# Kernel tuning notes

Hardware: AMD Instinct MI355X
Metric: run time of the kernel (lower is better)

The kernel has to match this reference:

```python
import jax, jax.numpy as jnp
import numpy as np

DEPTH, DIM, HEADS, DIM_HEAD, NBF, MULT = 2, 512, 8, 64, 256, 4
INNER = HEADS * DIM_HEAD


def layernorm(x, g, b, eps=1e-5):
    mu = jnp.mean(x, axis=-1, keepdims=True)
    var = jnp.mean((x - mu) ** 2, axis=-1, keepdims=True)
    return (x - mu) * jax.lax.rsqrt(var + eps) * g + b


def softmax_kernel(data, proj, is_query, eps=1e-4):
    # data: [b,h,n,d], proj: [m,d]  -> phi: [b,h,n,m]  (FAVOR+ positive features)
    d = data.shape[-1]
    normalizer = d ** -0.25
    ratio = proj.shape[0] ** -0.5
    data_dash = jnp.einsum('bhnd,md->bhnm', data * normalizer, proj)
    diag = jnp.sum(data ** 2, axis=-1, keepdims=True) * 0.5 * (normalizer ** 2)
    if is_query:
        m = jnp.max(data_dash, axis=-1, keepdims=True)
    else:
        m = jnp.max(data_dash, axis=(-2, -1), keepdims=True)
    m = jax.lax.stop_gradient(m)
    return ratio * (jnp.exp(data_dash - diag - m) + eps)


def setup_inputs() -> dict:
    key = jax.random.key(0)
    ks = jax.random.split(key, 16)
    s = 0.02
    B, N = 4, 8192
    inp = {
        'x': jax.random.normal(ks[0], (B, N, DIM), jnp.float32),
        'ln1_g': jnp.ones((DEPTH, DIM), jnp.float32),
        'ln1_b': jnp.zeros((DEPTH, DIM), jnp.float32),
        'ln2_g': jnp.ones((DEPTH, DIM), jnp.float32),
        'ln2_b': jnp.zeros((DEPTH, DIM), jnp.float32),
        'Wq': jax.random.normal(ks[1], (DEPTH, DIM, INNER), jnp.float32) * s,
        'bq': jnp.zeros((DEPTH, INNER), jnp.float32),
        'Wk': jax.random.normal(ks[2], (DEPTH, DIM, INNER), jnp.float32) * s,
        'bk': jnp.zeros((DEPTH, INNER), jnp.float32),
        'Wv': jax.random.normal(ks[3], (DEPTH, DIM, INNER), jnp.float32) * s,
        'bv': jnp.zeros((DEPTH, INNER), jnp.float32),
        'Wo': jax.random.normal(ks[4], (DEPTH, INNER, DIM), jnp.float32) * s,
        'bo': jnp.zeros((DEPTH, DIM), jnp.float32),
        'proj': jax.random.normal(ks[5], (DEPTH, NBF, DIM_HEAD), jnp.float32),
        'W1': jax.random.normal(ks[6], (DEPTH, DIM, DIM * MULT), jnp.float32) * s,
        'b1': jnp.zeros((DEPTH, DIM * MULT), jnp.float32),
        'W2': jax.random.normal(ks[7], (DEPTH, DIM * MULT, DIM), jnp.float32) * s,
        'b2': jnp.zeros((DEPTH, DIM), jnp.float32),
    }
    return inp


def reference(x, ln1_g, ln1_b, ln2_g, ln2_b, Wq, bq, Wk, bk, Wv, bv, Wo, bo, proj, W1, b1, W2, b2):
    B, N, D = x.shape
    for i in range(DEPTH):
        # --- PreLayerNorm + FAVOR+ self-attention, residual ---
        y = layernorm(x, ln1_g[i], ln1_b[i])
        q = (y @ Wq[i] + bq[i]).reshape(B, N, HEADS, DIM_HEAD).transpose(0, 2, 1, 3)
        k = (y @ Wk[i] + bk[i]).reshape(B, N, HEADS, DIM_HEAD).transpose(0, 2, 1, 3)
        v = (y @ Wv[i] + bv[i]).reshape(B, N, HEADS, DIM_HEAD).transpose(0, 2, 1, 3)
        qp = softmax_kernel(q, proj[i], True)   # [b,h,n,m]
        kp = softmax_kernel(k, proj[i], False)  # [b,h,n,m]
        # non-causal linear attention: O(n*m*d) instead of O(n^2)
        k_sum = kp.sum(axis=2)                               # [b,h,m]
        d_inv = 1.0 / jnp.einsum('bhnm,bhm->bhn', qp, k_sum)
        ctx = jnp.einsum('bhnm,bhnd->bhmd', kp, v)           # [b,h,m,d]
        o = jnp.einsum('bhmd,bhnm,bhn->bhnd', ctx, qp, d_inv)
        o = o.transpose(0, 2, 1, 3).reshape(B, N, INNER)
        x = x + o @ Wo[i] + bo[i]
        # --- PreLayerNorm + FeedForward (GELU), residual ---
        y = layernorm(x, ln2_g[i], ln2_b[i])
        h = jax.nn.gelu(y @ W1[i] + b1[i], approximate=False)
        x = x + h @ W2[i] + b2[i]
    return x
```

## Files before the change

### kernel.cpp

```cpp
#include <hip/hip_runtime.h>
#include <math.h>

#define DIMX 512
#define HEADS 8
#define DHEAD 64
#define NBFX 256
#define FFD 2048
#define NBX 4
#define SEQ 8192
#define TOK (NBX*SEQ)
#define NBH (NBX*HEADS)
#define VROWS 80
#define NCHUNK 16
#define BK 64

typedef unsigned short u16;
typedef __attribute__((ext_vector_type(8))) short short8;
typedef __attribute__((ext_vector_type(4))) float f32x4;

__device__ __forceinline__ float bf2f(u16 x){ return __uint_as_float(((unsigned)x)<<16); }
__device__ __forceinline__ u16 f2bf(float f){
  unsigned u=__float_as_uint(f);
  return (u16)((u + 0x7FFFu + ((u>>16)&1u))>>16);
}
__device__ __forceinline__ void gload16(const void* g, void* l){
  __builtin_amdgcn_global_load_lds((const __attribute__((address_space(1))) void*)g,
                                   (__attribute__((address_space(3))) void*)l, 16, 0, 0);
}
__device__ __forceinline__ float gelu_f(float v){
  float x=v*0.70710678118654752f;
  float ax=fabsf(x);
  float t=1.0f/(1.0f+0.3275911f*ax);
  float p=t*(0.254829592f+t*(-0.284496736f+t*(1.421413741f+t*(-1.453152027f+t*1.061405429f))));
  float erfv=1.0f-p*__expf(-ax*ax);
  erfv=(x<0.0f)? -erfv : erfv;
  return 0.5f*v*(1.0f+erfv);
}

#define FENCE asm volatile(""::: "memory")
#define BAR() do{ FENCE; __builtin_amdgcn_s_barrier(); FENCE; }while(0)

__global__ void copy_f32(const float4* __restrict__ s, float4* __restrict__ d, int n4){
  int i=blockIdx.x*blockDim.x+threadIdx.x;
  if(i<n4) d[i]=s[i];
}
__global__ void conv_proj(const float* __restrict__ p, u16* __restrict__ o, int n){
  int i=blockIdx.x*blockDim.x+threadIdx.x;
  if(i<n) o[i]=f2bf(p[i]*0.35355339059327373f);
}
__global__ void convT(const float* __restrict__ src, u16* __restrict__ dst, int K, int Ncol){
  __shared__ float t[32][33];
  int k0=blockIdx.y*32, n0=blockIdx.x*32;
  int tx=threadIdx.x, ty=threadIdx.y;
  for(int i=ty;i<32;i+=8) t[i][tx]=src[(size_t)(k0+i)*Ncol + n0+tx];
  __syncthreads();
  for(int i=ty;i<32;i+=8) dst[(size_t)(n0+i)*K + k0+tx]=f2bf(t[tx][i]);
}
__global__ void fill_vt(u16* __restrict__ vt){
  int i=blockIdx.x*blockDim.x+threadIdx.x;
  int n=i&(SEQ-1); int r=(i>>13)&15; int bh=i>>17;
  vt[((size_t)bh*VROWS + 64 + r)*SEQ + n] = (r==0)? (u16)0x3F80 : (u16)0;
}
__global__ void pack_bias(const float* __restrict__ bq, const float* __restrict__ bk,
                          const float* __restrict__ bv, float* __restrict__ o){
  int i=blockIdx.x*blockDim.x+threadIdx.x;
  int l=i/1536, c=i-l*1536;
  const float* s=(c<512)? bq : ((c<1024)? bk : bv);
  o[i]=s[l*512 + (c&511)];
}

__global__ __launch_bounds__(256) void ln_k(const float* __restrict__ x, const float* __restrict__ g,
                                            const float* __restrict__ b, u16* __restrict__ y){
  const int row=blockIdx.x*4 + (threadIdx.x>>6);
  const int ln=threadIdx.x&63;
  const float* xr=x+(size_t)row*DIMX;
  float4 v0=*(const float4*)&xr[ln*8];
  float4 v1=*(const float4*)&xr[ln*8+4];
  float v[8]={v0.x,v0.y,v0.z,v0.w,v1.x,v1.y,v1.z,v1.w};
  float s=0;
  #pragma unroll
  for(int e=0;e<8;e++) s+=v[e];
  #pragma unroll
  for(int m=1;m<64;m<<=1) s+=__shfl_xor(s,m);
  const float mean=s*(1.0f/DIMX);
  float s2=0;
  #pragma unroll
  for(int e=0;e<8;e++){ v[e]-=mean; s2+=v[e]*v[e]; }
  #pragma unroll
  for(int m=1;m<64;m<<=1) s2+=__shfl_xor(s2,m);
  const float rs=rsqrtf(s2*(1.0f/DIMX)+1e-5f);
  u16* yr=y+(size_t)row*DIMX+ln*8;
  u16 pk[8];
  #pragma unroll
  for(int e=0;e<8;e++) pk[e]=f2bf(v[e]*rs*g[ln*8+e]+b[ln*8+e]);
  uint4 pv;
  pv.x=(unsigned)pk[0]|((unsigned)pk[1]<<16); pv.y=(unsigned)pk[2]|((unsigned)pk[3]<<16);
  pv.z=(unsigned)pk[4]|((unsigned)pk[5]<<16); pv.w=(unsigned)pk[6]|((unsigned)pk[7]<<16);
  *(uint4*)yr=pv;
}

#define MFMA16(MH,BF,NH) do{                                                             \
  __builtin_amdgcn_s_setprio(1);                                                         \
  _Pragma("unroll") for(int kk_=0;kk_<2;kk_++)                                           \
    _Pragma("unroll") for(int i_=0;i_<4;i_++)                                            \
      _Pragma("unroll") for(int j_=0;j_<2;j_++)                                          \
        acc[MH][i_][NH][j_]=__builtin_amdgcn_mfma_f32_16x16x32_bf16(af[i_][kk_],BF[j_][kk_],acc[MH][i_][NH][j_],0,0,0); \
  __builtin_amdgcn_s_setprio(0);                                                         \
}while(0)

#define STG(T,HALF,ISB,BUF) do{ if((T)<nt){                                              \
  gload16(gp[ISB][HALF][0]+(size_t)(T)*BK, &lds[BUF][ISB][(HALF)*128 +    wv*8][0]);     \
  gload16(gp[ISB][HALF][1]+(size_t)(T)*BK, &lds[BUF][ISB][(HALF)*128 + 64+wv*8][0]); } }while(0)

#define LDA(BUF,MH) do{                                                                  \
  _Pragma("unroll") for(int i_=0;i_<4;i_++)                                              \
    _Pragma("unroll") for(int kk_=0;kk_<2;kk_++)                                         \
      af[i_][kk_]=*(const short8*)((const u16*)lds[BUF][0] + aoffs[MH][i_][kk_]); }while(0)

#define LDB(BF,BUF,NH) do{                                                               \
  _Pragma("unroll") for(int j_=0;j_<2;j_++)                                              \
    _Pragma("unroll") for(int kk_=0;kk_<2;kk_++)                                         \
      BF[j_][kk_]=*(const short8*)((const u16*)lds[BUF][1] + boffs[NH][j_][kk_]); }while(0)

#define TILE(T,BUF,OBUF) do{                                                             \
  LDB(bf0,BUF,0); LDA(BUF,0);                                                            \
  STG((T)+1,1,0,OBUF);                                                                   \
  BAR(); MFMA16(0,bf0,0); BAR();                                                         \
  LDB(bf1,BUF,1);                                                                        \
  STG((T)+1,1,1,OBUF);                                                                   \
  BAR(); MFMA16(0,bf1,1); BAR();                                                         \
  LDA(BUF,1);                                                                            \
  STG((T)+2,0,1,BUF);                                                                    \
  BAR(); MFMA16(1,bf0,0); BAR();                                                         \
  STG((T)+2,0,0,BUF);                                                                    \
  BAR(); MFMA16(1,bf1,1);                                                                \
  if((T)+2<nt) asm volatile("s_waitcnt vmcnt(4)":::"memory");                            \
  else         asm volatile("s_waitcnt vmcnt(0)":::"memory");                            \
  BAR();                                                                                 \
}while(0)

template<int EPI,int K>
__global__ __launch_bounds__(512,2) void gemm256(const u16* __restrict__ A, const u16* __restrict__ Bt,
                                                 const float* __restrict__ bias, void* __restrict__ outp,
                                                 u16* __restrict__ out2, int Ncol){
  constexpr int nt=K/BK;
  __shared__ u16 lds[2][2][256][64];
  const int tid=threadIdx.x, wv=tid>>6, ln=tid&63;
  const int wr=wv>>2, wc=wv&3;
  const int gx=gridDim.x, gy=gridDim.y;
  const int P=blockIdx.y*gx+blockIdx.x;
  const int band=gy>>3;
  const int xcd=P&7, sI=P>>3;
  const int by=xcd*band + (sI - (sI/band)*band);
  const int bx=sI/band;
  const int m0=by*256, n0=bx*256;
  f32x4 acc[2][4][2][2]={};

  const u16* gp[2][2][2];
  #pragma unroll
  for(int isB=0;isB<2;isB++)
    #pragma unroll
    for(int half=0;half<2;half++)
      #pragma unroll
      for(int s=0;s<2;s++){
        int G=s*512+wv*64+ln;
        int arow=half*128+(G>>3), g=G&7;
        const u16* src=isB? Bt:A;
        int b0=isB? n0:m0;
        gp[isB][half][s]=src+(size_t)(b0+arow)*K+((g^(arow&7))<<3);
      }
  int aoffs[2][4][2], boffs[2][2][2];
  #pragma unroll
  for(int mh=0;mh<2;mh++)
    #pragma unroll
    for(int i=0;i<4;i++){
      int row=wr*128+mh*64+i*16+(ln&15);
      #pragma unroll
      for(int kk=0;kk<2;kk++)
        aoffs[mh][i][kk]=row*64+((((kk*4+(ln>>4)))^(row&7))<<3);
    }
  #pragma unroll
  for(int nh=0;nh<2;nh++)
    #pragma unroll
    for(int j=0;j<2;j++){
      int row=wc*64+nh*32+j*16+(ln&15);
      #pragma unroll
      for(int kk=0;kk<2;kk++)
        boffs[nh][j][kk]=row*64+((((kk*4+(ln>>4)))^(row&7))<<3);
    }

  short8 af[4][2], bf0[2][2], bf1[2][2];

  STG(0,0,0,0); STG(0,1,0,0); STG(0,0,1,0); STG(0,1,1,0);
  STG(1,0,1,1); STG(1,0,0,1);
  asm volatile("s_waitcnt vmcnt(4)":::"memory");
  BAR();

  #pragma unroll 1
  for(int t=0;t<nt;t+=2){
    TILE(t,0,1);
    TILE(t+1,1,0);
  }

  #pragma unroll
  for(int mh=0;mh<2;mh++)
  #pragma unroll
  for(int i=0;i<4;i++)
  #pragma unroll
  for(int nh=0;nh<2;nh++)
  #pragma unroll
  for(int j=0;j<2;j++){
    const int row=m0+wr*128+mh*64+i*16+(ln>>4)*4;
    const int col=n0+wc*64+nh*32+j*16+(ln&15);
    const float bv=bias[col];
    const f32x4 a=acc[mh][i][nh][j];
    if constexpr(EPI==0){
      if(col<1024){
        u16* o=(u16*)outp + (size_t)(col>>9)*TOK*DIMX + (col&511);
        #pragma unroll
        for(int r=0;r<4;r++) o[(size_t)(row+r)*DIMX]=f2bf(a[r]+bv);
      } else {
        const int hd=col-1024, h_=hd>>6, d_=hd&63, b_=row>>13, nn=row&(SEQ-1);
        u16 pk[4];
        #pragma unroll
        for(int r=0;r<4;r++) pk[r]=f2bf(a[r]+bv);
        uint2 pv; pv.x=(unsigned)pk[0]|((unsigned)pk[1]<<16); pv.y=(unsigned)pk[2]|((unsigned)pk[3]<<16);
        *(uint2*)&out2[((size_t)(b_*HEADS+h_)*VROWS+d_)*SEQ+nn]=pv;
      }
    } else if constexpr(EPI==1){
      float* o=(float*)outp;
      #pragma unroll
      for(int r=0;r<4;r++){ size_t ix=(size_t)(row+r)*Ncol+col; o[ix]+=a[r]+bv; }
    } else {
      u16* o=(u16*)outp;
      #pragma unroll
      for(int r=0;r<4;r++)
        o[(size_t)(row+r)*Ncol+col]=f2bf(gelu_f(a[r]+bv));
    }
  }
}

__global__ __launch_bounds__(256) void vsum_k(const u16* __restrict__ vt, float* __restrict__ vs){
  const int gw=blockIdx.x*4 + (threadIdx.x>>6);
  const int ln=threadIdx.x&63;
  const int bh=gw/65, d=gw-bh*65;
  const u16* row=vt+((size_t)bh*VROWS+d)*SEQ;
  float s=0;
  for(int it=0;it<16;it++){
    short8 v=*(const short8*)&row[it*512+ln*8];
    #pragma unroll
    for(int e=0;e<8;e++) s+=bf2f((u16)v[e]);
  }
  #pragma unroll
  for(int m=1;m<64;m<<=1) s+=__shfl_xor(s,m);
  if(ln==0) vs[bh*80+d]=s;
}

__global__ __launch_bounds__(256) void kctx(const u16* __restrict__ kb, const u16* __restrict__ pj,
                                            const u16* __restrict__ vt,
                                            float* __restrict__ part, float* __restrict__ maxb){
  __shared__ u16 kl[64*64];
  __shared__ u16 vl[80*64];
  __shared__ u16 kp_l[128*64];
  __shared__ float dgl[64];
  const int kc=blockIdx.x, half=blockIdx.y, bh=blockIdx.z, b_=bh>>3, h_=bh&7;
  const int tid=threadIdx.x, wv=tid>>6, ln=tid&63;
  short8 pjf[2][2];
  #pragma unroll
  for(int i=0;i<2;i++)
    #pragma unroll
    for(int t=0;t<2;t++)
      pjf[i][t]=*(const short8*)&pj[(size_t)(half*128+wv*32+i*16+(ln&15))*DHEAD + t*32 + (ln>>4)*8];
  f32x4 ctx[2][5]={};
  float m_run=-3.0e38f;
  const u16* vbh=vt+(size_t)bh*VROWS*SEQ;
  for(int s=0;s<8;s++){
    const int n0s=kc*512+s*64;
    const u16* kg=kb+((size_t)(b_*SEQ+n0s))*DIMX + h_*DHEAD;
    #pragma unroll
    for(int cc=0;cc<2;cc++){
      int c=cc*256+wv*64+ln; int t=c>>3, g=c&7;
      gload16(kg+(size_t)t*DIMX+((g^(t&7))*8), &kl[(size_t)(cc*256+wv*64)*8]);
    }
    #pragma unroll
    for(int cc=0;cc<2;cc++){
      int c=cc*256+wv*64+ln; int d=c>>3, g=c&7;
      gload16(vbh+(size_t)d*SEQ+n0s+((g^(d&7))*8), &vl[(size_t)(cc*256+wv*64)*8]);
    }
    if(wv<2){
      int c=512+wv*64+ln; int d=c>>3, g=c&7;
      gload16(vbh+(size_t)d*SEQ+n0s+((g^(d&7))*8), &vl[(size_t)(512+wv*64)*8]);
    }
    __syncthreads();
    if(tid<64){
      float ss=0;
      #pragma unroll
      for(int gg=0;gg<8;gg++){
        short8 kv=*(const short8*)&kl[tid*64 + ((gg+tid)&7)*8];
        #pragma unroll
        for(int e=0;e<8;e++){ float x=bf2f((u16)kv[e]); ss+=x*x; }
      }
      dgl[tid]=ss*0.0625f;
    }
    __syncthreads();
    f32x4 dd[2][4]={};
    #pragma unroll
    for(int tk=0;tk<2;tk++)
      #pragma unroll
      for(int j=0;j<4;j++){
        short8 bk_=*(const short8*)&kl[(j*16+(ln&15))*64 + (((tk*4+(ln>>4))^(ln&7))<<3)];
        #pragma unroll
        for(int i=0;i<2;i++)
          dd[i][j]=__builtin_amdgcn_mfma_f32_16x16x32_bf16(pjf[i][tk],bk_,dd[i][j],0,0,0);
      }
    float mt=-3.0e38f;
    #pragma unroll
    for(int i=0;i<2;i++)
      #pragma unroll
      for(int j=0;j<4;j++)
        #pragma unroll
        for(int r=0;r<4;r++) mt=fmaxf(mt,dd[i][j][r]);
    #pragma unroll
    for(int m=1;m<64;m<<=1) mt=fmaxf(mt,__shfl_xor(mt,m));
    if(mt>m_run){
      float sc=__expf(m_run-mt);
      #pragma unroll
      for(int i=0;i<2;i++)
        #pragma unroll
        for(int j2=0;j2<5;j2++) ctx[i][j2]*=sc;
      m_run=mt;
    }
    #pragma unroll
    for(int j=0;j<4;j++){
      const float dgn=dgl[j*16+(ln&15)];
      #pragma unroll
      for(int i=0;i<2;i++)
        #pragma unroll
        for(int r=0;r<4;r++){
          int m_l=wv*32+i*16+(ln>>4)*4+r;
          float E=__expf(dd[i][j][r]-dgn-m_run);
          kp_l[m_l*64 + (((j*2+((ln>>3)&1))^(m_l&7))<<3) + (ln&7)]=f2bf(E);
        }
    }
    #pragma unroll
    for(int tk=0;tk<2;tk++){
      short8 af2[2];
      #pragma unroll
      for(int i=0;i<2;i++)
        af2[i]=*(const short8*)&kp_l[(wv*32+i*16+(ln&15))*64 + (((tk*4+(ln>>4))^(ln&7))<<3)];
      #pragma unroll
      for(int j2=0;j2<5;j2++){
        short8 bf2=*(const short8*)&vl[(j2*16+(ln&15))*64 + (((tk*4+(ln>>4))^(ln&7))<<3)];
        #pragma unroll
        for(int i=0;i<2;i++)
          ctx[i][j2]=__builtin_amdgcn_mfma_f32_16x16x32_bf16(af2[i],bf2,ctx[i][j2],0,0,0);
      }
    }
    __syncthreads();
  }
  float* po=part + ((size_t)(bh*NCHUNK+kc))*(256*80) + (size_t)half*128*80;
  #pragma unroll
  for(int i=0;i<2;i++)
    #pragma unroll
    for(int j2=0;j2<5;j2++)
      #pragma unroll
      for(int r=0;r<4;r++)
        po[(size_t)(wv*32+i*16+(ln>>4)*4+r)*80 + j2*16+(ln&15)]=ctx[i][j2][r];
  if(ln==0) maxb[bh*128 + kc*8 + half*4 + wv]=m_run;
}

__global__ __launch_bounds__(256) void ctx_reduce(const float* __restrict__ part, const float* __restrict__ maxb,
                                                  const float* __restrict__ vs,
                                                  u16* __restrict__ ctxT, float* __restrict__ ksum){
  __shared__ float mx_s[128];
  __shared__ float sc_s[NCHUNK];
  const int mseg=blockIdx.x, bh=blockIdx.y, tid=threadIdx.x;
  if(tid<128) mx_s[tid]=maxb[(size_t)bh*128+tid];
  __syncthreads();
  float km=-3.0e38f;
  for(int i=0;i<128;i++) km=fmaxf(km,mx_s[i]);
  const int m0=mseg*32;
  const int half=m0>>7, wvv=(m0&127)>>5;
  if(tid<NCHUNK) sc_s[tid]=__expf(mx_s[tid*8+half*4+wvv]-km);
  __syncthreads();
  for(int rep=0;rep<10;rep++){
    int idx=rep*256+tid;
    int mo=idx/80, d=idx-mo*80;
    int m=m0+mo;
    float s=0;
    #pragma unroll
    for(int c=0;c<NCHUNK;c++)
      s+=sc_s[c]*part[((size_t)(bh*NCHUNK+c))*(256*80) + (size_t)m*80 + d];
    float vsd=(d<=64)? vs[bh*80+d] : 0.0f;
    float val=0.0625f*(s + 1e-4f*vsd);
    if(d<64)       ctxT[((size_t)bh*64+d)*NBFX + m]=f2bf(val);
    else if(d==64) ksum[bh*NBFX+m]=val;
  }
}

__global__ void csum_k(const u16* __restrict__ ctxT, const float* __restrict__ ksum, float* __restrict__ cs){
  const int bh=blockIdx.x, t=threadIdx.x;
  if(t<64){
    const u16* r=ctxT+((size_t)bh*64+t)*NBFX;
    float s=0;
    for(int m=0;m<NBFX;m+=8){
      short8 v=*(const short8*)&r[m];
      #pragma unroll
      for(int e=0;e<8;e++) s+=bf2f((u16)v[e]);
    }
    cs[bh*80+t]=s;
  } else if(t==64){
    float s=0;
    for(int m=0;m<NBFX;m++) s+=ksum[bh*NBFX+m];
    cs[bh*80+64]=s;
  }
}

__global__ __launch_bounds__(256) void q_fused(const u16* __restrict__ qb, const u16* __restrict__ pj,
                                               const u16* __restrict__ ctxT, const float* __restrict__ ksum,
                                               const float* __restrict__ cs, u16* __restrict__ ob){
  __shared__ u16 ql[64*64];
  __shared__ u16 qpl[64*136];
  __shared__ float dgs[64];
  __shared__ float mred[4*64], dred[4*64];
  __shared__ float ff_s[64], dinv_s[64];
  const int bh=blockIdx.y, b_=bh>>3, h_=bh&7;
  const int n0=blockIdx.x*64;
  const int tid=threadIdx.x, wv=tid>>6, ln=tid&63;
  const u16* qg=qb+((size_t)(b_*SEQ+n0))*DIMX + h_*DHEAD;
  #pragma unroll
  for(int cc=0;cc<2;cc++){
    int c=cc*256+wv*64+ln; int t=c>>3, g=c&7;
    gload16(qg+(size_t)t*DIMX+((g^(t&7))*8), &ql[(size_t)(cc*256+wv*64)*8]);
  }
  short8 pjf[2][2][2];
  float ks[2][2][4];
  #pragma unroll
  for(int h=0;h<2;h++)
    #pragma unroll
    for(int i=0;i<2;i++){
      #pragma unroll
      for(int t=0;t<2;t++)
        pjf[h][i][t]=*(const short8*)&pj[(size_t)(h*128+wv*32+i*16+(ln&15))*DHEAD + t*32 + (ln>>4)*8];
      #pragma unroll
      for(int r=0;r<4;r++)
        ks[h][i][r]=ksum[bh*NBFX + h*128+wv*32+i*16+(ln>>4)*4+r];
    }
  const float KS=cs[bh*80+64];
  __syncthreads();
  if(tid<64){
    float ss=0;
    #pragma unroll
    for(int gg=0;gg<8;gg++){
      short8 kv=*(const short8*)&ql[tid*64 + ((gg+tid)&7)*8];
      #pragma unroll
      for(int e=0;e<8;e++){ float x=bf2f((u16)kv[e]); ss+=x*x; }
    }
    dgs[tid]=ss*0.0625f;
  }
  __syncthreads();
  float mxp[4]={-3.0e38f,-3.0e38f,-3.0e38f,-3.0e38f};
  float dnp[4]={0,0,0,0};
  f32x4 oc[4]={};
  const u16* cb=ctxT+(size_t)bh*64*NBFX;
  #pragma unroll
  for(int h=0;h<2;h++){
    #pragma unroll
    for(int j=0;j<4;j++){
      f32x4 dq[2]={};
      #pragma unroll
      for(int tk=0;tk<2;tk++){
        short8 bq=*(const short8*)&ql[(j*16+(ln&15))*64 + (((tk*4+(ln>>4))^(ln&7))<<3)];
        #pragma unroll
        for(int i=0;i<2;i++)
          dq[i]=__builtin_amdgcn_mfma_f32_16x16x32_bf16(pjf[h][i][tk],bq,dq[i],0,0,0);
      }
      const float dgn=dgs[j*16+(ln&15)];
      #pragma unroll
      for(int i=0;i<2;i++)
        #pragma unroll
        for(int r=0;r<4;r++){
          float d_=dq[i][r];
          mxp[j]=fmaxf(mxp[j],d_);
          float E=__expf(d_-dgn);
          dnp[j]+=E*ks[h][i][r];
          qpl[(j*16+(ln&15))*136 + wv*32+i*16+(ln>>4)*4+r]=f2bf(E);
        }
    }
    __syncthreads();
    #pragma unroll
    for(int mk2=0;mk2<4;mk2++){
      short8 aq=*(const short8*)&cb[(size_t)(wv*16+(ln&15))*NBFX + h*128 + mk2*32 + (ln>>4)*8];
      #pragma unroll
      for(int j2=0;j2<4;j2++){
        short8 bqp=*(const short8*)&qpl[(j2*16+(ln&15))*136 + mk2*32 + (ln>>4)*8];
        oc[j2]=__builtin_amdgcn_mfma_f32_16x16x32_bf16(aq,bqp,oc[j2],0,0,0);
      }
    }
    __syncthreads();
  }
  #pragma unroll
  for(int j=0;j<4;j++){
    #pragma unroll
    for(int msk=16;msk<64;msk<<=1){
      mxp[j]=fmaxf(mxp[j],__shfl_xor(mxp[j],msk));
      dnp[j]+=__shfl_xor(dnp[j],msk);
    }
  }
  if(ln<16){
    #pragma unroll
    for(int j=0;j<4;j++){ mred[wv*64+j*16+ln]=mxp[j]; dred[wv*64+j*16+ln]=dnp[j]; }
  }
  __syncthreads();
  if(tid<64){
    float mx=fmaxf(fmaxf(mred[tid],mred[64+tid]),fmaxf(mred[128+tid],mred[192+tid]));
    float dn=dred[tid]+dred[64+tid]+dred[128+tid]+dred[192+tid];
    float f=1e-4f*__expf(mx);
    ff_s[tid]=f;
    dinv_s[tid]=1.0f/(dn + f*KS);
  }
  __syncthreads();
  float csr[4];
  #pragma unroll
  for(int r=0;r<4;r++) csr[r]=cs[bh*80 + wv*16+(ln>>4)*4+r];
  u16* og=ob+((size_t)(b_*SEQ+n0))*DIMX + h_*DHEAD;
  #pragma unroll
  for(int j2=0;j2<4;j2++){
    int n=j2*16+(ln&15);
    float f=ff_s[n], di=dinv_s[n];
    u16 pk[4];
    #pragma unroll
    for(int r=0;r<4;r++) pk[r]=f2bf((oc[j2][r]+f*csr[r])*di);
    uint2 pv; pv.x=(unsigned)pk[0]|((unsigned)pk[1]<<16); pv.y=(unsigned)pk[2]|((unsigned)pk[3]<<16);
    *(uint2*)&og[(size_t)n*DIMX + wv*16+(ln>>4)*4]=pv;
  }
}

static constexpr size_t SZ_ACT=(size_t)TOK*DIMX*2;
static constexpr size_t O_Y=0, O_Q=SZ_ACT, O_K=2*SZ_ACT;
static constexpr size_t O_VT=3*SZ_ACT;
static constexpr size_t SZ_VT=(size_t)NBH*VROWS*SEQ*2;
static constexpr size_t O_PART=O_VT+SZ_VT;
static constexpr size_t SZ_PART=(size_t)NBH*NCHUNK*256*80*4;
static constexpr size_t O_CTXT=O_PART+SZ_PART;
static constexpr size_t SZ_CTXT=(size_t)NBH*64*NBFX*2;
static constexpr size_t O_KSUM=O_CTXT+SZ_CTXT;
static constexpr size_t SZ_KSUM=(size_t)NBH*NBFX*4;
static constexpr size_t O_MAX=O_KSUM+SZ_KSUM;
static constexpr size_t SZ_MAX=(size_t)NBH*128*4;
static constexpr size_t O_VSUM=O_MAX+SZ_MAX;
static constexpr size_t SZ_VSUM=(size_t)NBH*80*4;
static constexpr size_t O_CS=O_VSUM+SZ_VSUM;
static constexpr size_t SZ_CS=(size_t)NBH*80*4;
static constexpr size_t O_WQKV=O_CS+SZ_CS;
static constexpr size_t SZ_WQKV=(size_t)2*1536*DIMX*2;
static constexpr size_t O_WOT=O_WQKV+SZ_WQKV;
static constexpr size_t SZ_W=(size_t)2*DIMX*DIMX*2;
static constexpr size_t O_W1T=O_WOT+SZ_W;
static constexpr size_t SZ_W1=(size_t)2*FFD*DIMX*2;
static constexpr size_t O_W2T=O_W1T+SZ_W1;
static constexpr size_t O_PJ=O_W2T+SZ_W1;
static constexpr size_t O_QKVB=O_PJ+(size_t)2*NBFX*DHEAD*2;
static constexpr size_t WS_END=O_QKVB+(size_t)2*1536*4;

extern "C" void kernel_launch(void* const* d_in, const int* in_sizes, int n_in,
                              void* d_out, int out_size, void* d_ws, size_t ws_size,
                              hipStream_t stream){
  (void)in_sizes;(void)n_in;(void)out_size;
  const float* xin =(const float*)d_in[0];
  const float* ln1g=(const float*)d_in[1];
  const float* ln1b=(const float*)d_in[2];
  const float* ln2g=(const float*)d_in[3];
  const float* ln2b=(const float*)d_in[4];
  const float* Wq=(const float*)d_in[5];
  const float* bq=(const float*)d_in[6];
  const float* Wk=(const float*)d_in[7];
  const float* bk=(const float*)d_in[8];
  const float* Wv=(const float*)d_in[9];
  const float* bv=(const float*)d_in[10];
  const float* Wo=(const float*)d_in[11];
  const float* bo=(const float*)d_in[12];
  const float* proj=(const float*)d_in[13];
  const float* W1=(const float*)d_in[14];
  const float* b1=(const float*)d_in[15];
  const float* W2=(const float*)d_in[16];
  const float* b2=(const float*)d_in[17];
  float* xout=(float*)d_out;

  copy_f32<<<(TOK*DIMX/4)/256,256,0,stream>>>((const float4*)xin,(float4*)xout, TOK*DIMX/4);
  if(ws_size < WS_END) return;

  char* ws=(char*)d_ws;
  u16* ybuf =(u16*)(ws+O_Y);
  u16* qbuf =(u16*)(ws+O_Q);
  u16* kbuf =(u16*)(ws+O_K);
  u16* vtb  =(u16*)(ws+O_VT);
  float* partb=(float*)(ws+O_PART);
  u16* ctxtb=(u16*)(ws+O_CTXT);
  float* ksumb=(float*)(ws+O_KSUM);
  float* maxb=(float*)(ws+O_MAX);
  float* vsumb=(float*)(ws+O_VSUM);
  float* csb=(float*)(ws+O_CS);
  u16* wqkvt=(u16*)(ws+O_WQKV);
  u16* wot=(u16*)(ws+O_WOT);
  u16* w1t=(u16*)(ws+O_W1T); u16* w2t=(u16*)(ws+O_W2T);
  u16* pjb=(u16*)(ws+O_PJ);
  float* qkvb=(float*)(ws+O_QKVB);
  u16* hbuf=(u16*)(ws+O_Q);

  for(int l=0;l<2;l++){
    size_t wo=(size_t)l*DIMX*DIMX;
    convT<<<dim3(16,16),dim3(32,8),0,stream>>>(Wq+wo, wqkvt+(size_t)(l*1536+   0)*DIMX, DIMX, DIMX);
    convT<<<dim3(16,16),dim3(32,8),0,stream>>>(Wk+wo, wqkvt+(size_t)(l*1536+ 512)*DIMX, DIMX, DIMX);
    convT<<<dim3(16,16),dim3(32,8),0,stream>>>(Wv+wo, wqkvt+(size_t)(l*1536+1024)*DIMX, DIMX, DIMX);
    convT<<<dim3(16,16),dim3(32,8),0,stream>>>(Wo+wo, wot+wo, DIMX, DIMX);
    size_t w1o=(size_t)l*DIMX*FFD;
    convT<<<dim3(64,16),dim3(32,8),0,stream>>>(W1+w1o, w1t+w1o, DIMX, FFD);
    convT<<<dim3(16,64),dim3(32,8),0,stream>>>(W2+w1o, w2t+w1o, FFD, DIMX);
  }
  conv_proj<<<(2*NBFX*DHEAD)/256,256,0,stream>>>(proj, pjb, 2*NBFX*DHEAD);
  pack_bias<<<12,256,0,stream>>>(bq,bk,bv,qkvb);

  for(int l=0;l<2;l++){
    const u16* wqkvt_l=wqkvt+(size_t)l*1536*DIMX;
    const u16* wot_l=wot+(size_t)l*DIMX*DIMX;
    const u16* w1t_l=w1t+(size_t)l*DIMX*FFD;
    const u16* w2t_l=w2t+(size_t)l*DIMX*FFD;
    const u16* pj_l =pjb+(size_t)l*NBFX*DHEAD;
    const float* qkvb_l=qkvb+(size_t)l*1536;

    ln_k<<<TOK/4,256,0,stream>>>(xout, ln1g+l*DIMX, ln1b+l*DIMX, ybuf);
    fill_vt<<<(NBH*16*SEQ)/256,256,0,stream>>>(vtb);
    gemm256<0,512><<<dim3(6,128),512,0,stream>>>(ybuf, wqkvt_l, qkvb_l, qbuf, vtb, 1536);
    vsum_k<<<520,256,0,stream>>>(vtb, vsumb);
    kctx<<<dim3(NCHUNK,2,32),256,0,stream>>>(kbuf, pj_l, vtb, partb, maxb);
    ctx_reduce<<<dim3(8,32),256,0,stream>>>(partb, maxb, vsumb, ctxtb, ksumb);
    csum_k<<<32,256,0,stream>>>(ctxtb, ksumb, csb);
    q_fused<<<dim3(128,32),256,0,stream>>>(qbuf, pj_l, ctxtb, ksumb, csb, ybuf);
    gemm256<1,512><<<dim3(2,128),512,0,stream>>>(ybuf, wot_l, bo+l*DIMX, xout, nullptr, DIMX);
    ln_k<<<TOK/4,256,0,stream>>>(xout, ln2g+l*DIMX, ln2b+l*DIMX, ybuf);
    gemm256<2,512><<<dim3(8,128),512,0,stream>>>(ybuf, w1t_l, b1+l*FFD, hbuf, nullptr, FFD);
    gemm256<1,2048><<<dim3(2,128),512,0,stream>>>(hbuf, w2t_l, b2+l*DIMX, xout, nullptr, DIMX);
  }
}
```

Before: 1.049 ms.

## Replace pipelined 256x256 GEMM with simple 128x128 single-buffered GEMM

Swaps the double-buffered, software-pipelined 512-thread GEMM with 256x256 tiles for a straightforward 256-thread kernel with 128x128 tiles. Each K-step loads both tiles directly into LDS, syncs, runs the MFMAs and syncs again. Launch grids are doubled in each dimension to match. This gains simplicity and more resident blocks, but gives up the overlap of global loads with MFMA work and halves data reuse per tile.

```diff
diff --git a/kernel.cpp b/kernel.cpp
--- a/kernel.cpp
+++ b/kernel.cpp
@@ -12,7 +12,6 @@
 #define NBH (NBX*HEADS)
 #define VROWS 80
 #define NCHUNK 16
-#define BK 64
 
 typedef unsigned short u16;
 typedef __attribute__((ext_vector_type(8))) short short8;
@@ -36,9 +35,6 @@
   erfv=(x<0.0f)? -erfv : erfv;
   return 0.5f*v*(1.0f+erfv);
 }
-
-#define FENCE asm volatile(""::: "memory")
-#define BAR() do{ FENCE; __builtin_amdgcn_s_barrier(); FENCE; }while(0)
 
 __global__ void copy_f32(const float4* __restrict__ s, float4* __restrict__ d, int n4){
   int i=blockIdx.x*blockDim.x+threadIdx.x;
@@ -99,121 +95,67 @@
   *(uint4*)yr=pv;
 }
 
-#define MFMA16(MH,BF,NH) do{                                                             \
-  __builtin_amdgcn_s_setprio(1);                                                         \
-  _Pragma("unroll") for(int kk_=0;kk_<2;kk_++)                                           \
-    _Pragma("unroll") for(int i_=0;i_<4;i_++)                                            \
-      _Pragma("unroll") for(int j_=0;j_<2;j_++)                                          \
-        acc[MH][i_][NH][j_]=__builtin_amdgcn_mfma_f32_16x16x32_bf16(af[i_][kk_],BF[j_][kk_],acc[MH][i_][NH][j_],0,0,0); \
-  __builtin_amdgcn_s_setprio(0);                                                         \
-}while(0)
-
-#define STG(T,HALF,ISB,BUF) do{ if((T)<nt){                                              \
-  gload16(gp[ISB][HALF][0]+(size_t)(T)*BK, &lds[BUF][ISB][(HALF)*128 +    wv*8][0]);     \
-  gload16(gp[ISB][HALF][1]+(size_t)(T)*BK, &lds[BUF][ISB][(HALF)*128 + 64+wv*8][0]); } }while(0)
-
-#define LDA(BUF,MH) do{                                                                  \
-  _Pragma("unroll") for(int i_=0;i_<4;i_++)                                              \
-    _Pragma("unroll") for(int kk_=0;kk_<2;kk_++)                                         \
-      af[i_][kk_]=*(const short8*)((const u16*)lds[BUF][0] + aoffs[MH][i_][kk_]); }while(0)
-
-#define LDB(BF,BUF,NH) do{                                                               \
-  _Pragma("unroll") for(int j_=0;j_<2;j_++)                                              \
-    _Pragma("unroll") for(int kk_=0;kk_<2;kk_++)                                         \
-      BF[j_][kk_]=*(const short8*)((const u16*)lds[BUF][1] + boffs[NH][j_][kk_]); }while(0)
-
-#define TILE(T,BUF,OBUF) do{                                                             \
-  LDB(bf0,BUF,0); LDA(BUF,0);                                                            \
-  STG((T)+1,1,0,OBUF);                                                                   \
-  BAR(); MFMA16(0,bf0,0); BAR();                                                         \
-  LDB(bf1,BUF,1);                                                                        \
-  STG((T)+1,1,1,OBUF);                                                                   \
-  BAR(); MFMA16(0,bf1,1); BAR();                                                         \
-  LDA(BUF,1);                                                                            \
-  STG((T)+2,0,1,BUF);                                                                    \
-  BAR(); MFMA16(1,bf0,0); BAR();                                                         \
-  STG((T)+2,0,0,BUF);                                                                    \
-  BAR(); MFMA16(1,bf1,1);                                                                \
-  if((T)+2<nt) asm volatile("s_waitcnt vmcnt(4)":::"memory");                            \
-  else         asm volatile("s_waitcnt vmcnt(0)":::"memory");                            \
-  BAR();                                                                                 \
-}while(0)
-
 template<int EPI,int K>
-__global__ __launch_bounds__(512,2) void gemm256(const u16* __restrict__ A, const u16* __restrict__ Bt,
-                                                 const float* __restrict__ bias, void* __restrict__ outp,
-                                                 u16* __restrict__ out2, int Ncol){
-  constexpr int nt=K/BK;
-  __shared__ u16 lds[2][2][256][64];
+__global__ __launch_bounds__(256) void gemm128(const u16* __restrict__ A, const u16* __restrict__ Bt,
+                                               const float* __restrict__ bias, void* __restrict__ outp,
+                                               u16* __restrict__ out2, int Ncol){
+  __shared__ u16 As[128*64];
+  __shared__ u16 Bs[128*64];
   const int tid=threadIdx.x, wv=tid>>6, ln=tid&63;
-  const int wr=wv>>2, wc=wv&3;
+  const int wr=wv>>1, wc=wv&1;
   const int gx=gridDim.x, gy=gridDim.y;
   const int P=blockIdx.y*gx+blockIdx.x;
   const int band=gy>>3;
   const int xcd=P&7, sI=P>>3;
   const int by=xcd*band + (sI - (sI/band)*band);
   const int bx=sI/band;
-  const int m0=by*256, n0=bx*256;
-  f32x4 acc[2][4][2][2]={};
-
-  const u16* gp[2][2][2];
-  #pragma unroll
-  for(int isB=0;isB<2;isB++)
-    #pragma unroll
-    for(int half=0;half<2;half++)
-      #pragma unroll
-      for(int s=0;s<2;s++){
-        int G=s*512+wv*64+ln;
-        int arow=half*128+(G>>3), g=G&7;
-        const u16* src=isB? Bt:A;
-        int b0=isB? n0:m0;
-        gp[isB][half][s]=src+(size_t)(b0+arow)*K+((g^(arow&7))<<3);
-      }
-  int aoffs[2][4][2], boffs[2][2][2];
-  #pragma unroll
-  for(int mh=0;mh<2;mh++)
+  const int m0=by*128, n0=bx*128;
+  f32x4 acc[4][4]={};
+  const u16* Ab=A+(size_t)m0*K;
+  const u16* Bb=Bt+(size_t)n0*K;
+
+  for(int kt=0;kt<K;kt+=64){
+    #pragma unroll
+    for(int it=0;it<4;it++){
+      int c=it*256+wv*64+ln; int row=c>>3, g=c&7;
+      size_t so=(size_t)row*K+kt+((g^(row&7))<<3);
+      gload16(Ab+so, &As[(size_t)(it*256+wv*64)*8]);
+      gload16(Bb+so, &Bs[(size_t)(it*256+wv*64)*8]);
+    }
+    __syncthreads();
+    short8 af[4][2], bfr[4][2];
     #pragma unroll
     for(int i=0;i<4;i++){
-      int row=wr*128+mh*64+i*16+(ln&15);
-      #pragma unroll
-      for(int kk=0;kk<2;kk++)
-        aoffs[mh][i][kk]=row*64+((((kk*4+(ln>>4)))^(row&7))<<3);
-    }
-  #pragma unroll
-  for(int nh=0;nh<2;nh++)
-    #pragma unroll
-    for(int j=0;j<2;j++){
-      int row=wc*64+nh*32+j*16+(ln&15);
-      #pragma unroll
-      for(int kk=0;kk<2;kk++)
-        boffs[nh][j][kk]=row*64+((((kk*4+(ln>>4)))^(row&7))<<3);
-    }
-
-  short8 af[4][2], bf0[2][2], bf1[2][2];
-
-  STG(0,0,0,0); STG(0,1,0,0); STG(0,0,1,0); STG(0,1,1,0);
-  STG(1,0,1,1); STG(1,0,0,1);
-  asm volatile("s_waitcnt vmcnt(4)":::"memory");
-  BAR();
-
-  #pragma unroll 1
-  for(int t=0;t<nt;t+=2){
-    TILE(t,0,1);
-    TILE(t+1,1,0);
-  }
-
-  #pragma unroll
-  for(int mh=0;mh<2;mh++)
+      int row=wr*64+i*16+(ln&15);
+      #pragma unroll
+      for(int tk=0;tk<2;tk++)
+        af[i][tk]=*(const short8*)&As[row*64 + (((tk*4+(ln>>4))^(row&7))<<3)];
+    }
+    #pragma unroll
+    for(int j=0;j<4;j++){
+      int row=wc*64+j*16+(ln&15);
+      #pragma unroll
+      for(int tk=0;tk<2;tk++)
+        bfr[j][tk]=*(const short8*)&Bs[row*64 + (((tk*4+(ln>>4))^(row&7))<<3)];
+    }
+    #pragma unroll
+    for(int tk=0;tk<2;tk++)
+      #pragma unroll
+      for(int i=0;i<4;i++)
+        #pragma unroll
+        for(int j=0;j<4;j++)
+          acc[i][j]=__builtin_amdgcn_mfma_f32_16x16x32_bf16(af[i][tk],bfr[j][tk],acc[i][j],0,0,0);
+    __syncthreads();
+  }
+
   #pragma unroll
   for(int i=0;i<4;i++)
   #pragma unroll
-  for(int nh=0;nh<2;nh++)
-  #pragma unroll
-  for(int j=0;j<2;j++){
-    const int row=m0+wr*128+mh*64+i*16+(ln>>4)*4;
-    const int col=n0+wc*64+nh*32+j*16+(ln&15);
+  for(int j=0;j<4;j++){
+    const int row=m0+wr*64+i*16+(ln>>4)*4;
+    const int col=n0+wc*64+j*16+(ln&15);
     const float bv=bias[col];
-    const f32x4 a=acc[mh][i][nh][j];
+    const f32x4 a=acc[i][j];
     if constexpr(EPI==0){
       if(col<1024){
         u16* o=(u16*)outp + (size_t)(col>>9)*TOK*DIMX + (col&511);
@@ -631,15 +573,15 @@
 
     ln_k<<<TOK/4,256,0,stream>>>(xout, ln1g+l*DIMX, ln1b+l*DIMX, ybuf);
     fill_vt<<<(NBH*16*SEQ)/256,256,0,stream>>>(vtb);
-    gemm256<0,512><<<dim3(6,128),512,0,stream>>>(ybuf, wqkvt_l, qkvb_l, qbuf, vtb, 1536);
+    gemm128<0,512><<<dim3(12,256),256,0,stream>>>(ybuf, wqkvt_l, qkvb_l, qbuf, vtb, 1536);
     vsum_k<<<520,256,0,stream>>>(vtb, vsumb);
     kctx<<<dim3(NCHUNK,2,32),256,0,stream>>>(kbuf, pj_l, vtb, partb, maxb);
     ctx_reduce<<<dim3(8,32),256,0,stream>>>(partb, maxb, vsumb, ctxtb, ksumb);
     csum_k<<<32,256,0,stream>>>(ctxtb, ksumb, csb);
     q_fused<<<dim3(128,32),256,0,stream>>>(qbuf, pj_l, ctxtb, ksumb, csb, ybuf);
-    gemm256<1,512><<<dim3(2,128),512,0,stream>>>(ybuf, wot_l, bo+l*DIMX, xout, nullptr, DIMX);
+    gemm128<1,512><<<dim3(4,256),256,0,stream>>>(ybuf, wot_l, bo+l*DIMX, xout, nullptr, DIMX);
     ln_k<<<TOK/4,256,0,stream>>>(xout, ln2g+l*DIMX, ln2b+l*DIMX, ybuf);
-    gemm256<2,512><<<dim3(8,128),512,0,stream>>>(ybuf, w1t_l, b1+l*FFD, hbuf, nullptr, FFD);
-    gemm256<1,2048><<<dim3(2,128),512,0,stream>>>(hbuf, w2t_l, b2+l*DIMX, xout, nullptr, DIMX);
-  }
-}
+    gemm128<2,512><<<dim3(16,256),256,0,stream>>>(ybuf, w1t_l, b1+l*FFD, hbuf, nullptr, FFD);
+    gemm128<1,2048><<<dim3(4,256),256,0,stream>>>(hbuf, w2t_l, b2+l*DIMX, xout, nullptr, DIMX);
+  }
+}
```

Result: slower. 1.159 ms (+10.5%).
